# Performance work log

Hardware: AMD Instinct MI355X
Metric: run time of the kernel (lower is better)

The kernel has to match this reference:

```python
import jax, jax.numpy as jnp
import numpy as np

PAD = 2  # kernel_height // 2 for kernel_height=5


def earth_pad2d(x, ph, pw):
    # circular pad in longitude (last dim), zero pad in latitude (dim 2)
    if pw > 0:
        x = jnp.concatenate([x[..., -pw:], x, x[..., :pw]], axis=-1)
    if ph > 0:
        x = jnp.pad(x, ((0, 0), (0, 0), (ph, ph), (0, 0)))
    return x


def earth_wrap2d(x, w, pad):
    # fold circular overhang of a transposed-conv output back onto width w
    core = x[..., pad:pad + w]
    rw = x.shape[-1] - pad - w  # right overhang (stride-1... here 1)
    core = core.at[..., :rw].add(x[..., pad + w:])
    core = core.at[..., w - pad:].add(x[..., :pad])
    return core


def _conv(x, w, b, stride):
    # torch Conv2d, weight [Cout, Cin, 1, k], VALID padding, stride (1, stride)
    y = jax.lax.conv_general_dilated(x, w, (1, stride), 'VALID',
                                     dimension_numbers=('NCHW', 'OIHW', 'NCHW'))
    return y + b[None, :, None, None]


def _convT(x, w, stride):
    # torch ConvTranspose2d (no bias), weight [Cin, Cout, 1, k], padding 0
    k = w.shape[-1]
    wr = jnp.transpose(jnp.flip(w, axis=(2, 3)), (1, 0, 2, 3))  # -> [Cout, Cin, 1, k]
    return jax.lax.conv_general_dilated(x, wr, (1, 1),
                                        [(0, 0), (k - 1, k - 1)],
                                        lhs_dilation=(1, stride),
                                        dimension_numbers=('NCHW', 'OIHW', 'NCHW'))


def _edge(x, d, p):
    return x[:, :, -p:, :] if d == 1 else x[:, :, :p, :]


def _set_edge(x, d, p, v):
    return x.at[:, :, -p:, :].set(v) if d == 1 else x.at[:, :, :p, :].set(v)


def _forward(strips, wi, wo):
    strips_pad = [earth_pad2d(s, PAD, PAD) for s in strips]
    # center strip inner edges from the adjacent coarser strips (to_inners[0])
    for d in (-1, 1):
        a = _edge(strips[2 + d], -d, PAD)
        a = _convT(a, wi[0], 2)
        a = earth_wrap2d(a, strips[2].shape[3], 2)
        a = earth_pad2d(a, 0, PAD)
        strips_pad[2] = _set_edge(strips_pad[2], d, PAD, a)
    # outer strips: far edge from next coarser (to_inners), near edge from finer (to_outers)
    for mi in (1, 2):
        for d in (-1, 1):
            idx = 2 + d * mi
            sp = strips_pad[idx]
            if mi + 1 <= 2:
                o = _edge(strips[2 + d * (mi + 1)], -d, PAD)
                o = _convT(o, wi[mi], 2)
                o = earth_wrap2d(o, strips[idx].shape[3], 2)
                o = earth_pad2d(o, 0, PAD)
                sp = _set_edge(sp, d, PAD, o)
            en = _edge(strips[2 + d * (mi - 1)], d, PAD)
            en = earth_pad2d(en, 0, 2)
            en = _conv(en, wo[mi - 1][0], wo[mi - 1][1], 2)
            en = earth_pad2d(en, 0, PAD)
            sp = _set_edge(sp, -d, PAD, en)
            strips_pad[idx] = sp
    return tuple(strips_pad)


def setup_inputs():
    key = jax.random.key(0)
    ks = jax.random.split(key, 11)
    B, C, W = 1, 256, 1440
    shapes = [(B, C, 30, W // 4), (B, C, 60, W // 2), (B, C, 180, W),
              (B, C, 60, W // 2), (B, C, 30, W // 4)]
    d = {}
    for i, sh in enumerate(shapes):
        d['s%d' % i] = jax.random.normal(ks[i], sh, dtype=jnp.float32)
    scale = 0.03
    d['wi0'] = jax.random.normal(ks[5], (C, C, 1, 5), dtype=jnp.float32) * scale
    d['wi1'] = jax.random.normal(ks[6], (C, C, 1, 5), dtype=jnp.float32) * scale
    d['wo0'] = jax.random.normal(ks[7], (C, C, 1, 5), dtype=jnp.float32) * scale
    d['bo0'] = jax.random.normal(ks[8], (C,), dtype=jnp.float32) * 0.01
    d['wo1'] = jax.random.normal(ks[9], (C, C, 1, 5), dtype=jnp.float32) * scale
    d['bo1'] = jax.random.normal(ks[10], (C,), dtype=jnp.float32) * 0.01
    return d


def reference(s0, s1, s2, s3, s4, wi0, wi1, wo0, bo0, wo1, bo1):
    return _forward([s0, s1, s2, s3, s4], [wi0, wi1], [(wo0, bo0), (wo1, bo1)])
```

## Files before the change

kernel.cpp:

```cpp
#include <hip/hip_runtime.h>


struct ConvJob {
  const float* x; const float* wt; const float* bias; float* out;
  int Hin, Win, r0, Hout, Wcore, h0;
};
struct ConvParams { ConvJob j[8]; };

struct CopyParams {
  const float* in0; const float* in1; const float* in2; const float* in3; const float* in4;
  float* o0; float* o1; float* o2; float* o3; float* o4;
};

struct WTParams { const float* src[4]; float* dst[4]; };

__global__ __launch_bounds__(256) void transpose_all_kernel(WTParams p) {
  int b = blockIdx.x;
  int which = b / 1280;
  int idx = (b - which * 1280) * 256 + threadIdx.x;
  int hi = idx >> 10;
  int icq = hi / 5;
  int k = hi - icq * 5;
  int lo = idx & 1023;
  int oc = lo >> 2;
  int icr = lo & 3;
  int ic = icq * 4 + icr;
  const float* s = p.src[which];
  float v = (which < 2) ? s[(ic * 256 + oc) * 5 + k] : s[(oc * 256 + ic) * 5 + k];
  p.dst[which][idx] = v;
}


template <int NOUT>
__device__ __forceinline__ void epilogue_row(const ConvJob& jb, int g0, int t, int r,
                                             const float* acc, float* xs) {
  __syncthreads();
#pragma unroll
  for (int i = 0; i < NOUT; ++i) xs[i * 257 + t] = acc[i];
  __syncthreads();
  constexpr int SL = NOUT / 2;
  constexpr int OCR = 256 / SL;
  const int Hout = jb.Hout;
  const int Wop = jb.Wcore + 4;
#pragma unroll
  for (int q = 0; q < SL; ++q) {
    int oc = (t / SL) + q * OCR;
    int s = t & (SL - 1);
    float2 v = make_float2(xs[(2 * s) * 257 + oc], xs[(2 * s + 1) * 257 + oc]);
    *(float2*)(jb.out + ((size_t)(oc * Hout + jb.h0 + r)) * Wop + 2 + g0 + 2 * s) = v;
  }
  float* orow = jb.out + ((size_t)(t * Hout + jb.h0 + r)) * Wop;
  if (g0 == 0) {
    orow[jb.Wcore + 2] = xs[0 * 257 + t];
    orow[jb.Wcore + 3] = xs[1 * 257 + t];
  }
  if (g0 + NOUT == jb.Wcore) {
    orow[0] = xs[(NOUT - 2) * 257 + t];
    orow[1] = xs[(NOUT - 1) * 257 + t];
  }
}

template <int NOUT, int NCC, bool TR>
__device__ __forceinline__ void conv2(const ConvJob jb, int tile, int t, float* xs,
                                      float bv) {
  const int Win = jb.Win;
  int g0 = tile * NOUT;
  int base0 = TR ? (g0 >> 1) - 1 : 2 * g0 - 2;

#pragma unroll
  for (int r = 0; r < 2; ++r) {
    const float* xrow = jb.x + ((size_t)(t * jb.Hin + jb.r0 + r)) * Win;
#pragma unroll
    for (int cc = 0; cc < NCC; ++cc) {
      int col = base0 + cc;
      col += (col < 0) ? Win : 0;
      col -= (col >= Win) ? Win : 0;
      xs[(r * NCC + cc) * 256 + t] = xrow[col];
    }
  }
  __syncthreads();

  float a0[NOUT], a1[NOUT];
#pragma unroll
  for (int i = 0; i < NOUT; ++i) { a0[i] = bv; a1[i] = bv; }

  const float* wq = jb.wt + t * 4;
  float4 wv[5], wn[5];
#pragma unroll
  for (int k = 0; k < 5; ++k) wv[k] = *(const float4*)(wq + (size_t)k * 1024);

#pragma unroll 1
  for (int icq = 0; icq < 64; ++icq) {
    if (icq < 63) {
#pragma unroll
      for (int k = 0; k < 5; ++k)
        wn[k] = *(const float4*)(wq + (size_t)((icq + 1) * 5 + k) * 1024);
    }
    int ic0 = icq * 4;
#pragma unroll
    for (int cc = 0; cc < NCC; ++cc) {
      float4 x0 = *(const float4*)&xs[cc * 256 + ic0];
      float4 x1 = *(const float4*)&xs[(NCC + cc) * 256 + ic0];
#pragma unroll
      for (int i = 0; i < NOUT; ++i) {
        int k = TR ? (i + 4 - 2 * cc) : (cc - 2 * i);
        if (k >= 0 && k < 5) {
          float4 w = wv[k];
          a0[i] += w.x * x0.x + w.y * x0.y + w.z * x0.z + w.w * x0.w;
          a1[i] += w.x * x1.x + w.y * x1.y + w.z * x1.z + w.w * x1.w;
        }
      }
    }
    if (icq < 63) {
#pragma unroll
      for (int k = 0; k < 5; ++k) wv[k] = wn[k];
    }
  }

  epilogue_row<NOUT>(jb, g0, t, 0, a0, xs);
  __syncthreads();
  epilogue_row<NOUT>(jb, g0, t, 1, a1, xs);
}

__global__ __launch_bounds__(256, 2) void conv_kernel(ConvParams p) {
  __shared__ float xs[2 * 19 * 256];
  int bx = blockIdx.x;
  int t = threadIdx.x;
  int job = bx & 7;
  int tile = bx >> 3;
  const ConvJob jb = p.j[job];
  switch (job >> 1) {
    case 0: conv2<16, 10, true>(jb, tile, t, xs, 0.f); break;
    case 1: conv2<8, 6, true>(jb, tile, t, xs, 0.f); break;
    case 2: conv2<8, 19, false>(jb, tile, t, xs, jb.bias[t]); break;
    default: conv2<4, 11, false>(jb, tile, t, xs, jb.bias[t]); break;
  }
}


__device__ __forceinline__ float4 pack4(float2 a, float2 b) {
  return make_float4(a.x, a.y, b.x, b.y);
}

template <int H, int W>
__device__ __forceinline__ void copy_row(const float* __restrict__ in,
                                         float* __restrict__ out, int rl, int lane) {
  constexpr int CORE = W / 4;
  int c = rl / H;
  const float* src = in + (size_t)rl * W;
  float* dst = out + (size_t)(rl + c * 4 + 2) * (W + 4);
  int w4 = 1 + lane;
  while (w4 < CORE) {
    int w4b = w4 + 64;
    float2 a0 = *(const float2*)(src + w4 * 4 - 2);
    float2 b0 = *(const float2*)(src + w4 * 4);
    if (w4b < CORE) {
      float2 a1 = *(const float2*)(src + w4b * 4 - 2);
      float2 b1 = *(const float2*)(src + w4b * 4);
      *(float4*)(dst + w4 * 4) = pack4(a0, b0);
      *(float4*)(dst + w4b * 4) = pack4(a1, b1);
    } else {
      *(float4*)(dst + w4 * 4) = pack4(a0, b0);
    }
    w4 += 128;
  }
  if (lane == 0) {
    float2 E = *(const float2*)(src + W - 2);
    float2 F = *(const float2*)(src);
    float4 v = pack4(E, F);
    *(float4*)(dst) = v;
    *(float4*)(dst + W) = v;
  }
}

__device__ __forceinline__ void zero_row(const CopyParams& p, int z, int lane) {
  int strip = z >> 9, cr = z & 511, c = cr >> 1, r = cr & 1;
  float* dst = strip ? p.o4 + (size_t)(c * 34 + 32 + r) * 364
                     : p.o0 + (size_t)(c * 34 + r) * 364;
  for (int w4 = lane; w4 < 91; w4 += 64)
    *(float4*)(dst + w4 * 4) = make_float4(0.f, 0.f, 0.f, 0.f);
}

__device__ __forceinline__ void do_row(const CopyParams& p, int gid, int lane) {
  if (gid < 46080)      copy_row<180, 1440>(p.in2, p.o2, gid, lane);
  else if (gid < 61440) copy_row<60, 720>(p.in1, p.o1, gid - 46080, lane);
  else if (gid < 76800) copy_row<60, 720>(p.in3, p.o3, gid - 61440, lane);
  else if (gid < 84480) copy_row<30, 360>(p.in0, p.o0, gid - 76800, lane);
  else if (gid < 92160) copy_row<30, 360>(p.in4, p.o4, gid - 84480, lane);
  else                  zero_row(p, gid - 92160, lane);
}

__global__ __launch_bounds__(256, 8) void copy_kernel(CopyParams p) {
  int wid = blockIdx.x * 4 + (threadIdx.x >> 6);
  int lane = threadIdx.x & 63;
  for (int gid = wid; gid < 93184; gid += 8192) do_row(p, gid, lane);
}

extern "C" void kernel_launch(void* const* d_in, const int* in_sizes, int n_in,
                              void* d_out, int out_size, void* d_ws, size_t ws_size,
                              hipStream_t stream) {
  const float* s0 = (const float*)d_in[0];
  const float* s1 = (const float*)d_in[1];
  const float* s2 = (const float*)d_in[2];
  const float* s3 = (const float*)d_in[3];
  const float* s4 = (const float*)d_in[4];
  const float* wi0 = (const float*)d_in[5];
  const float* wi1 = (const float*)d_in[6];
  const float* wo0 = (const float*)d_in[7];
  const float* bo0 = (const float*)d_in[8];
  const float* wo1 = (const float*)d_in[9];
  const float* bo1 = (const float*)d_in[10];

  float* out = (float*)d_out;
  float* out0 = out;
  float* out1 = out + 3168256;
  float* out2 = out + 15030272;
  float* out3 = out + 83048448;
  float* out4 = out + 94910464;

  float* wt0 = (float*)d_ws;
  float* wt1 = wt0 + 327680;
  float* wt2 = wt1 + 327680;
  float* wt3 = wt2 + 327680;

  WTParams wp;
  wp.src[0] = wi0; wp.src[1] = wi1; wp.src[2] = wo0; wp.src[3] = wo1;
  wp.dst[0] = wt0; wp.dst[1] = wt1; wp.dst[2] = wt2; wp.dst[3] = wt3;
  transpose_all_kernel<<<5120, 256, 0, stream>>>(wp);

  ConvParams cp;
  cp.j[0] = {s1, wt0, nullptr, out2,  60,  720,  58, 184, 1440,   0};
  cp.j[1] = {s3, wt0, nullptr, out2,  60,  720,   0, 184, 1440, 182};
  cp.j[2] = {s0, wt1, nullptr, out1,  30,  360,  28,  64,  720,   0};
  cp.j[3] = {s4, wt1, nullptr, out3,  30,  360,   0,  64,  720,  62};
  cp.j[4] = {s2, wt2, bo0,     out1, 180, 1440,   0,  64,  720,  62};
  cp.j[5] = {s2, wt2, bo0,     out3, 180, 1440, 178,  64,  720,   0};
  cp.j[6] = {s1, wt3, bo1,     out0,  60,  720,   0,  34,  360,  32};
  cp.j[7] = {s3, wt3, bo1,     out4,  60,  720,  58,  34,  360,   0};
  conv_kernel<<<720, 256, 0, stream>>>(cp);

  CopyParams kp;
  kp.in0 = s0; kp.in1 = s1; kp.in2 = s2; kp.in3 = s3; kp.in4 = s4;
  kp.o0 = out0; kp.o1 = out1; kp.o2 = out2; kp.o3 = out3; kp.o4 = out4;
  copy_kernel<<<2048, 256, 0, stream>>>(kp);
}
```

Measured before the change: 370.0 us.

## Read conv inputs directly from global with uniform loads instead of LDS staging

```diff
diff --git a/kernel.cpp b/kernel.cpp
--- a/kernel.cpp
+++ b/kernel.cpp
@@ -64,57 +64,59 @@
 __device__ __forceinline__ void conv2(const ConvJob jb, int tile, int t, float* xs,
                                       float bv) {
   const int Win = jb.Win;
+  const int Hin = jb.Hin;
   int g0 = tile * NOUT;
   int base0 = TR ? (g0 >> 1) - 1 : 2 * g0 - 2;
-
-#pragma unroll
-  for (int r = 0; r < 2; ++r) {
-    const float* xrow = jb.x + ((size_t)(t * jb.Hin + jb.r0 + r)) * Win;
-#pragma unroll
-    for (int cc = 0; cc < NCC; ++cc) {
-      int col = base0 + cc;
-      col += (col < 0) ? Win : 0;
-      col -= (col >= Win) ? Win : 0;
-      xs[(r * NCC + cc) * 256 + t] = xrow[col];
-    }
-  }
-  __syncthreads();
+  bool edge = (base0 < 0) || (base0 + NCC - 1 >= Win);
 
   float a0[NOUT], a1[NOUT];
 #pragma unroll
   for (int i = 0; i < NOUT; ++i) { a0[i] = bv; a1[i] = bv; }
 
   const float* wq = jb.wt + t * 4;
-  float4 wv[5], wn[5];
-#pragma unroll
-  for (int k = 0; k < 5; ++k) wv[k] = *(const float4*)(wq + (size_t)k * 1024);
 
 #pragma unroll 1
   for (int icq = 0; icq < 64; ++icq) {
-    if (icq < 63) {
-#pragma unroll
-      for (int k = 0; k < 5; ++k)
-        wn[k] = *(const float4*)(wq + (size_t)((icq + 1) * 5 + k) * 1024);
-    }
-    int ic0 = icq * 4;
-#pragma unroll
-    for (int cc = 0; cc < NCC; ++cc) {
-      float4 x0 = *(const float4*)&xs[cc * 256 + ic0];
-      float4 x1 = *(const float4*)&xs[(NCC + cc) * 256 + ic0];
-#pragma unroll
-      for (int i = 0; i < NOUT; ++i) {
-        int k = TR ? (i + 4 - 2 * cc) : (cc - 2 * i);
-        if (k >= 0 && k < 5) {
-          float4 w = wv[k];
-          a0[i] += w.x * x0.x + w.y * x0.y + w.z * x0.z + w.w * x0.w;
-          a1[i] += w.x * x1.x + w.y * x1.y + w.z * x1.z + w.w * x1.w;
+    float4 wv[5];
+#pragma unroll
+    for (int k = 0; k < 5; ++k)
+      wv[k] = *(const float4*)(wq + (size_t)(icq * 5 + k) * 1024);
+#pragma unroll
+    for (int j = 0; j < 4; ++j) {
+      int ic = icq * 4 + j;
+      const float* xr0 = jb.x + ((size_t)(ic * Hin + jb.r0)) * Win;
+      const float* xr1 = xr0 + Win;
+      float x0v[NCC], x1v[NCC];
+      if (!edge) {
+#pragma unroll
+        for (int cc = 0; cc < NCC; ++cc) {
+          x0v[cc] = xr0[base0 + cc];
+          x1v[cc] = xr1[base0 + cc];
+        }
+      } else {
+#pragma unroll
+        for (int cc = 0; cc < NCC; ++cc) {
+          int col = base0 + cc;
+          col += (col < 0) ? Win : 0;
+          col -= (col >= Win) ? Win : 0;
+          x0v[cc] = xr0[col];
+          x1v[cc] = xr1[col];
+        }
+      }
+#pragma unroll
+      for (int cc = 0; cc < NCC; ++cc) {
+#pragma unroll
+        for (int i = 0; i < NOUT; ++i) {
+          int k = TR ? (i + 4 - 2 * cc) : (cc - 2 * i);
+          if (k >= 0 && k < 5) {
+            float w = (j == 0) ? wv[k].x : (j == 1) ? wv[k].y : (j == 2) ? wv[k].z
+                                                                        : wv[k].w;
+            a0[i] += w * x0v[cc];
+            a1[i] += w * x1v[cc];
+          }
         }
       }
     }
-    if (icq < 63) {
-#pragma unroll
-      for (int k = 0; k < 5; ++k) wv[k] = wn[k];
-    }
   }
 
   epilogue_row<NOUT>(jb, g0, t, 0, a0, xs);
@@ -122,8 +124,8 @@
   epilogue_row<NOUT>(jb, g0, t, 1, a1, xs);
 }
 
-__global__ __launch_bounds__(256, 2) void conv_kernel(ConvParams p) {
-  __shared__ float xs[2 * 19 * 256];
+__global__ __launch_bounds__(256, 4) void conv_kernel(ConvParams p) {
+  __shared__ float xs[16 * 257];
   int bx = blockIdx.x;
   int t = threadIdx.x;
   int job = bx & 7;
```

Result: slower. 892.1 us (+141.1%).
